# Performance work log

Hardware: AMD Instinct MI355X
Metric: run time of the kernel (lower is better)

Reference implementation:

```python
import jax, jax.numpy as jnp
import numpy as np
from jax import lax

T_SCALE = 100
D_SCALE = 100
NUM_SAMPLE = 32
PER_BIN = 3
RATIO = 0.5


def _build_sample_mask(tscale=T_SCALE, dscale=D_SCALE, num_sample=NUM_SAMPLE, perbin=PER_BIN, ratio=RATIO):
    # Vectorized, bit-faithful port of BM_layer._get_interp1d_mask (incl. np.modf
    # semantics matching math.modf for negative samples).
    T, D = tscale, dscale
    total = num_sample * perbin
    s = np.arange(T, dtype=np.float64)[:, None, None]   # start index
    d = np.arange(D, dtype=np.float64)[None, :, None]   # duration index
    clen = d + 1.0
    xmin = s - ratio * clen
    plen = d + 2.0 * ratio * clen                        # sample_xmax - sample_xmin
    step = plen / (total - 1.0)
    ii = np.arange(total, dtype=np.float64)[None, None, :]
    samples = xmin + step * ii                           # [T_start, D, total]
    frac, down_f = np.modf(samples)                      # trunc-toward-zero, like math.modf
    down = down_f.astype(np.int64)
    up = np.ceil(samples).astype(np.int64)
    acc = np.zeros((T, D, num_sample, T), dtype=np.float64)  # [start, dur, bin, time]
    S, Dg, I = np.indices((T, D, total))
    Bn = I // perbin
    m = (down >= 0) & (down <= T - 1)
    np.add.at(acc, (S[m], Dg[m], Bn[m], down[m]), 1.0 - frac[m])
    m = (up >= 0) & (up <= T - 1)
    np.add.at(acc, (S[m], Dg[m], Bn[m], up[m]), frac[m])
    acc /= perbin
    valid = (np.arange(T)[:, None] + np.arange(D)[None, :]) < T  # start+dur < tscale
    acc *= valid[:, :, None, None]
    # torch layout: [time, sample, dur, start]
    return jnp.asarray(acc.transpose(3, 2, 1, 0).astype(np.float32))


def _conv2d(x, w, pad):
    return lax.conv_general_dilated(x, w, (1, 1), ((pad, pad), (pad, pad)),
                                    dimension_numbers=('NCHW', 'OIHW', 'NCHW'))


def setup_inputs() -> dict:
    key = jax.random.key(0)
    ks = jax.random.split(key, 8)
    B, C_in, T = 4, 256, T_SCALE

    def w(k, shape, fan_in):
        return jax.random.normal(k, shape, dtype=jnp.float32) * (1.0 / np.sqrt(fan_in))

    return {
        'x': jax.random.normal(ks[0], (B, C_in, T), dtype=jnp.float32),
        'w_rd': w(ks[1], (128, C_in, 3), C_in * 3),      'b_rd': jnp.zeros((128,), jnp.float32),
        'w3d': w(ks[2], (512, 128, NUM_SAMPLE), 128 * NUM_SAMPLE), 'b3d': jnp.zeros((512,), jnp.float32),
        'w2d': w(ks[3], (128, 512), 512),                 'b2d': jnp.zeros((128,), jnp.float32),
        'wf1': w(ks[4], (128, 128, 3, 3), 128 * 9),       'bf1': jnp.zeros((128,), jnp.float32),
        'wf2': w(ks[5], (128, 128, 3, 3), 128 * 9),       'bf2': jnp.zeros((128,), jnp.float32),
        'wf3': w(ks[6], (2, 128), 128),                   'bf3': jnp.zeros((2,), jnp.float32),
        'sample_mask': _build_sample_mask(),
    }


def reference(x, w_rd, b_rd, w3d, b3d, w2d, b2d, wf1, bf1, wf2, bf2, wf3, bf3, sample_mask):
    # reduce_dim: Conv1d(256->128, k=3, pad=1) + ReLU
    h = lax.conv_general_dilated(x, w_rd, (1,), ((1, 1),),
                                 dimension_numbers=('NCH', 'OIH', 'NCH'))
    h = jax.nn.relu(h + b_rd[None, :, None])                       # [B,128,T]
    # tensordot over time axis against fixed interpolation mask
    map_base = jnp.einsum('bct,tsdu->bcsdu', h, sample_mask)       # [B,128,32,D,T]
    # conv3d with kernel (32,1,1) stride (32,1,1) == contraction over (c, s)
    m3 = jax.nn.relu(jnp.einsum('bcsdu,ocs->bodu', map_base, w3d) + b3d[None, :, None, None])
    # 1x1 conv2d 512->128
    m2 = jax.nn.relu(jnp.einsum('bodu,ko->bkdu', m3, w2d) + b2d[None, :, None, None])
    # PEM.fc head
    f = jax.nn.relu(_conv2d(m2, wf1, 1) + bf1[None, :, None, None])
    f = jax.nn.relu(_conv2d(f, wf2, 1) + bf2[None, :, None, None])
    out = jax.nn.sigmoid(jnp.einsum('bchw,kc->bkhw', f, wf3) + bf3[None, :, None, None])
    return out  # [B, 2, D, T]
```

## Files before the change

### kernel.cpp

```cpp
#include <hip/hip_runtime.h>
#include <hip/hip_bf16.h>
#include <cstdint>
#include <cstddef>

static constexpr int B   = 4;
static constexpr int CIN = 256;
static constexpr int T   = 100;
static constexpr int D   = 100;
static constexpr int S   = 32;
static constexpr int C1  = 128;
static constexpr int DU  = D * T;

typedef __attribute__((ext_vector_type(8))) short bfv8;
typedef __attribute__((ext_vector_type(4))) short bfv4;
typedef __attribute__((ext_vector_type(4))) float fx4;
typedef unsigned short us;

static __device__ __forceinline__ unsigned short f2bf(float f) {
    unsigned int x = __float_as_uint(f);
    x += 0x7FFFu + ((x >> 16) & 1u);
    return (unsigned short)(x >> 16);
}
static __device__ __forceinline__ unsigned int pk2(float a, float b) {
    return (unsigned int)f2bf(a) | ((unsigned int)f2bf(b) << 16);
}

#define MFMA16(A, Bq, C) __builtin_amdgcn_mfma_f32_16x16x32_bf16((A), (Bq), (C), 0, 0, 0)

static __device__ __forceinline__ void gload16(const void* g, void* l) {
    __builtin_amdgcn_global_load_lds(
        (const __attribute__((address_space(1))) void*)g,
        (__attribute__((address_space(3))) void*)l, 16, 0, 0);
}

__global__ __launch_bounds__(256)
void kFront(const float* __restrict__ w3d, us* __restrict__ w3B,
            const float* __restrict__ w2d, us* __restrict__ w2b,
            const float* __restrict__ wf1, us* __restrict__ wfb1,
            const float* __restrict__ wf2, us* __restrict__ wfb2,
            const float* __restrict__ x,  const float* __restrict__ wrd,
            const float* __restrict__ brd, us* __restrict__ hT,
            const float* __restrict__ mask, us* __restrict__ maskW) {
    __shared__ float wl[2][CIN * 3];
    int bid = blockIdx.x;
    int t = threadIdx.x;
    if (bid < 8192) {
        int tid = bid * 256 + t;
        int c = tid & 127;
        int o = (tid >> 7) & 511;
        int s = tid >> 16;
        w3B[tid] = f2bf(w3d[(o * 128 + c) * 32 + s]);
        return;
    }
    if (bid < 8448) {
        int tid = (bid - 8192) * 256 + t;
        w2b[tid] = f2bf(w2d[tid]);
        return;
    }
    if (bid < 9024) {
        int tid = (bid - 8448) * 256 + t;
        int c   = tid & 127;
        int k   = (tid >> 7) & 127;
        int tap = tid >> 14;
        wfb1[tid] = f2bf(wf1[(size_t)(k * 128 + c) * 9 + tap]);
        return;
    }
    if (bid < 9600) {
        int tid = (bid - 9024) * 256 + t;
        int c   = tid & 127;
        int k   = (tid >> 7) & 127;
        int tap = tid >> 14;
        wfb2[tid] = f2bf(wf2[(size_t)(k * 128 + c) * 9 + tap]);
        return;
    }
    if (bid < 9856) {
        int j = bid - 9600;
        int b  = j >> 6;
        int op = j & 63;
        int half = t >> 7;
        int lt   = t & 127;
        int o = op * 2 + half;
        for (int i = lt; i < CIN * 3; i += 128)
            wl[half][i] = wrd[o * CIN * 3 + i];
        __syncthreads();
        int tt = lt;
        float val = 0.f;
        if (tt < T) {
            float acc = brd[o];
            const float* xb = x + (size_t)b * CIN * T;
            for (int c = 0; c < CIN; ++c) {
                float xm = (tt > 0)     ? xb[c * T + tt - 1] : 0.f;
                float x0 =                xb[c * T + tt];
                float xp = (tt < T - 1) ? xb[c * T + tt + 1] : 0.f;
                acc = fmaf(wl[half][c * 3 + 0], xm, acc);
                acc = fmaf(wl[half][c * 3 + 1], x0, acc);
                acc = fmaf(wl[half][c * 3 + 2], xp, acc);
            }
            val = fmaxf(acc, 0.f);
        }
        hT[((size_t)b * 128 + tt) * 128 + o] = f2bf(val);
        return;
    }
    {
        int mb = bid - 9856;
        int ut = mb % 7;
        int dq = (mb / 7) % 25;
        int s  = mb / 175;
        int dd = t >> 6;
        int l  = t & 63;
        int l15 = l & 15, lg = l >> 4;
        int u0 = ut * 16;
        int d0 = dq * 4;

        float fs1 = (float)(3 * s), fs2 = (float)(3 * s + 2);
        float pmin = 1e30f, pmax = -1e30f;
#pragma unroll
        for (int j = 0; j < 4; ++j) {
            float dj = (float)(d0 + j);
            float step = (2.f * dj + 1.f) * (1.f / 95.f);
            float xoff = -0.5f * (dj + 1.f);
            pmin = fminf(pmin, xoff + fs1 * step);
            pmax = fmaxf(pmax, xoff + fs2 * step);
        }
        float pminT = (float)u0 + pmin;
        float pmaxT = (float)(u0 + 15) + pmax;
        bool skip = (pminT > 100.01f) || (pmaxT < -1.01f);
        int t0 = (int)floorf(pminT) - 1;
        if (t0 < 0) t0 = 0;
        t0 &= ~3;
        if (t0 > 96) t0 = 96;

        int u = u0 + l15;
        int d = d0 + dd;
        float v[8];
#pragma unroll
        for (int j = 0; j < 8; ++j) {
            int tt = t0 + lg * 8 + j;
            v[j] = 0.f;
            if (!skip && tt < 100 && u < 100)
                v[j] = mask[(((size_t)tt * 32 + s) * 100 + d) * 100 + u];
        }
        uint4 pk;
        pk.x = pk2(v[0], v[1]); pk.y = pk2(v[2], v[3]);
        pk.z = pk2(v[4], v[5]); pk.w = pk2(v[6], v[7]);
        *(uint4*)(maskW + (size_t)mb * 2048 + t * 8) = pk;
    }
}

__global__ __launch_bounds__(256, 2)
void kQm(const us* __restrict__ w3B, const us* __restrict__ hT,
         us* __restrict__ QT) {
    int bid = blockIdx.x;
    int oh = bid & 1;
    int s  = (bid >> 1) & 31;
    int b  = bid >> 6;
    int tid = threadIdx.x;
    int w   = tid >> 6;
    int l   = tid & 63;
    int l15 = l & 15, lg = l >> 4;
    int obase = oh * 256 + w * 64;
    fx4 acc[4][8];
#pragma unroll
    for (int m = 0; m < 4; ++m)
#pragma unroll
        for (int n = 0; n < 8; ++n) acc[m][n] = (fx4){0.f, 0.f, 0.f, 0.f};

#pragma unroll
    for (int ks = 0; ks < 4; ++ks) {
        int kofs = ks * 32 + lg * 8;
        bfv8 a0 = *(const bfv8*)(w3B + (size_t)(s * 512 + obase + 0 * 16 + l15) * 128 + kofs);
        bfv8 a1 = *(const bfv8*)(w3B + (size_t)(s * 512 + obase + 1 * 16 + l15) * 128 + kofs);
        bfv8 a2 = *(const bfv8*)(w3B + (size_t)(s * 512 + obase + 2 * 16 + l15) * 128 + kofs);
        bfv8 a3 = *(const bfv8*)(w3B + (size_t)(s * 512 + obase + 3 * 16 + l15) * 128 + kofs);
#pragma unroll
        for (int n = 0; n < 8; ++n) {
            bfv8 bq = *(const bfv8*)(hT + (size_t)(b * 128 + n * 16 + l15) * 128 + kofs);
            acc[0][n] = MFMA16(a0, bq, acc[0][n]);
            acc[1][n] = MFMA16(a1, bq, acc[1][n]);
            acc[2][n] = MFMA16(a2, bq, acc[2][n]);
            acc[3][n] = MFMA16(a3, bq, acc[3][n]);
        }
    }
    us* outb = QT + (size_t)(b * 32 + s) * 512 * 128;
#pragma unroll
    for (int m = 0; m < 4; ++m)
#pragma unroll
        for (int n = 0; n < 8; ++n)
#pragma unroll
            for (int r = 0; r < 4; ++r) {
                int o = obase + m * 16 + lg * 4 + r;
                outb[(size_t)o * 128 + n * 16 + l15] = f2bf(acc[m][n][r]);
            }
}

__global__ __launch_bounds__(128, 4)
void kM3m(const us* __restrict__ maskW, const us* __restrict__ QT,
          const float* __restrict__ b3d, us* __restrict__ m3b) {
    __shared__ int sl[32];
    __shared__ int nsh;
    int bid = blockIdx.x;
    int x  = bid & 7;
    int b  = x >> 1;
    int ohalf = x & 1;
    int i  = bid >> 3;
    int dq = i / 14;
    int r2 = i % 14;
    int ut = r2 >> 1;
    int os = r2 & 1;
    int u0 = ut * 16;
    int d0 = dq * 4;
    int tid = threadIdx.x;
    int w   = tid >> 6;
    int l   = tid & 63;
    int l15 = l & 15, lg = l >> 4;
    int obase = ohalf * 256 + os * 128 + w * 64;

    if (tid < 64) {
        int s = tid;
        float fs1 = (float)(3 * s), fs2 = (float)(3 * s + 2);
        float pmin = 1e30f, pmax = -1e30f;
#pragma unroll
        for (int j = 0; j < 4; ++j) {
            float dj = (float)(d0 + j);
            float step = (2.f * dj + 1.f) * (1.f / 95.f);
            float xoff = -0.5f * (dj + 1.f);
            pmin = fminf(pmin, xoff + fs1 * step);
            pmax = fmaxf(pmax, xoff + fs2 * step);
        }
        float pminT = (float)u0 + pmin;
        float pmaxT = (float)(u0 + 15) + pmax;
        bool valid = (s < 32) && !((pminT > 100.01f) || (pmaxT < -1.01f));
        int t0 = (int)floorf(pminT) - 1;
        if (t0 < 0) t0 = 0;
        t0 &= ~3;
        if (t0 > 96) t0 = 96;
        unsigned long long mb = __ballot(valid);
        int rank = __popcll(mb & ((1ull << tid) - 1ull));
        if (valid) sl[rank] = (t0 << 8) | s;
        if (tid == 0) nsh = (int)__popcll(mb);
    }
    __syncthreads();
    int ns = nsh;

    fx4 acc[4][4];
#pragma unroll
    for (int m = 0; m < 4; ++m)
#pragma unroll
        for (int n = 0; n < 4; ++n) acc[m][n] = (fx4){0.f, 0.f, 0.f, 0.f};

    const us* QTb = QT + (size_t)b * 32 * 65536
                       + (size_t)(obase + l15) * 128 + lg * 8;
    const us* mwBase = maskW + (size_t)(dq * 7 + ut) * 2048 + l * 8;

    for (int si = 0; si < ns; ++si) {
        int pk = sl[si];
        int s_ = pk & 255, t0_ = pk >> 8;
        const us* mw = mwBase + (size_t)s_ * 358400;
        bfv8 A0 = *(const bfv8*)(mw);
        bfv8 A1 = *(const bfv8*)(mw + 512);
        bfv8 A2 = *(const bfv8*)(mw + 1024);
        bfv8 A3 = *(const bfv8*)(mw + 1536);
        const us* qs = QTb + (size_t)s_ * 65536 + t0_;
        bfv4 b0l = *(const bfv4*)(qs);        bfv4 b0h = *(const bfv4*)(qs + 4);
        bfv4 b1l = *(const bfv4*)(qs + 2048); bfv4 b1h = *(const bfv4*)(qs + 2052);
        bfv4 b2l = *(const bfv4*)(qs + 4096); bfv4 b2h = *(const bfv4*)(qs + 4100);
        bfv4 b3l = *(const bfv4*)(qs + 6144); bfv4 b3h = *(const bfv4*)(qs + 6148);
        bfv8 B0 = __builtin_shufflevector(b0l, b0h, 0, 1, 2, 3, 4, 5, 6, 7);
        bfv8 B1 = __builtin_shufflevector(b1l, b1h, 0, 1, 2, 3, 4, 5, 6, 7);
        bfv8 B2 = __builtin_shufflevector(b2l, b2h, 0, 1, 2, 3, 4, 5, 6, 7);
        bfv8 B3 = __builtin_shufflevector(b3l, b3h, 0, 1, 2, 3, 4, 5, 6, 7);
        __builtin_amdgcn_s_setprio(1);
        acc[0][0] = MFMA16(A0, B0, acc[0][0]);  acc[1][0] = MFMA16(A1, B0, acc[1][0]);
        acc[2][0] = MFMA16(A2, B0, acc[2][0]);  acc[3][0] = MFMA16(A3, B0, acc[3][0]);
        acc[0][1] = MFMA16(A0, B1, acc[0][1]);  acc[1][1] = MFMA16(A1, B1, acc[1][1]);
        acc[2][1] = MFMA16(A2, B1, acc[2][1]);  acc[3][1] = MFMA16(A3, B1, acc[3][1]);
        acc[0][2] = MFMA16(A0, B2, acc[0][2]);  acc[1][2] = MFMA16(A1, B2, acc[1][2]);
        acc[2][2] = MFMA16(A2, B2, acc[2][2]);  acc[3][2] = MFMA16(A3, B2, acc[3][2]);
        acc[0][3] = MFMA16(A0, B3, acc[0][3]);  acc[1][3] = MFMA16(A1, B3, acc[1][3]);
        acc[2][3] = MFMA16(A2, B3, acc[2][3]);  acc[3][3] = MFMA16(A3, B3, acc[3][3]);
        __builtin_amdgcn_s_setprio(0);
    }

#pragma unroll
    for (int dd = 0; dd < 4; ++dd) {
#pragma unroll
        for (int n = 0; n < 4; ++n) {
            int o = obase + n * 16 + l15;
            float bias = b3d[o];
#pragma unroll
            for (int r4 = 0; r4 < 4; ++r4) {
                int u = u0 + lg * 4 + r4;
                if (u < 100)
                    m3b[((size_t)b * DU + (d0 + dd) * 100 + u) * 512 + o] =
                        f2bf(fmaxf(acc[dd][n][r4] + bias, 0.f));
            }
        }
    }
}

__global__ __launch_bounds__(256, 4)
void kM2m(const us* __restrict__ m3b, const us* __restrict__ w2b,
          const float* __restrict__ b2d, us* __restrict__ m2b) {
    int blk  = blockIdx.x;
    int tile = blk % 157;
    int b    = blk / 157;
    int du0  = tile * 64;
    int tid = threadIdx.x;
    int w   = tid >> 6;
    int l   = tid & 63;
    int l15 = l & 15, lg = l >> 4;
    fx4 acc[8];
#pragma unroll
    for (int n = 0; n < 8; ++n) acc[n] = (fx4){0.f, 0.f, 0.f, 0.f};

    int dua = du0 + w * 16 + l15; if (dua > 9999) dua = 9999;
    const us* ap = m3b + ((size_t)b * DU + dua) * 512;
#pragma unroll 4
    for (int ks = 0; ks < 16; ++ks) {
        bfv8 a = *(const bfv8*)(ap + ks * 32 + lg * 8);
#pragma unroll
        for (int n = 0; n < 8; ++n) {
            bfv8 bq = *(const bfv8*)(w2b + (size_t)(n * 16 + l15) * 512 + ks * 32 + lg * 8);
            acc[n] = MFMA16(a, bq, acc[n]);
        }
    }
#pragma unroll
    for (int n = 0; n < 8; ++n) {
        int k = n * 16 + l15;
        float bias = b2d[k];
#pragma unroll
        for (int r = 0; r < 4; ++r) {
            int du = du0 + w * 16 + lg * 4 + r;
            if (du < DU)
                m2b[((size_t)b * DU + du) * 128 + k] = f2bf(fmaxf(acc[n][r] + bias, 0.f));
        }
    }
}

template<int HEAD>
__global__ __launch_bounds__(256, 2)
void kConvM(const us* __restrict__ fin, const us* __restrict__ wfb,
            const float* __restrict__ bf, us* __restrict__ fout,
            const float* __restrict__ wf3, const float* __restrict__ bf3,
            float* __restrict__ hout) {
    __shared__ us slab[6 * 18 * 128];
    __shared__ us wl2[2][8192];
    int blk = blockIdx.x;
    int ut = blk % 7;
    int dt = (blk / 7) % 25;
    int b  = blk / 175;
    int u0 = ut * 16, d0 = dt * 4;
    int tid = threadIdx.x;
    int w   = tid >> 6;
    int l   = tid & 63;
    int l15 = l & 15, lg = l >> 4;
    fx4 acc[8];
#pragma unroll
    for (int n = 0; n < 8; ++n) acc[n] = (fx4){0.f, 0.f, 0.f, 0.f};

#define STAGE_W(BUF, P)                                                        \
    {   const int tap_ = (P) >> 1, ch_ = (P) & 1;                              \
        const us* wsrc = wfb + (size_t)tap_ * 16384 + ch_ * 64;                \
        _Pragma("unroll")                                                      \
        for (int rr = 0; rr < 4; ++rr) {                                       \
            int seg = rr * 4 + w;                                              \
            int off = seg * 1024 + l * 16;                                     \
            int k_ = off >> 7, cb_ = off & 127;                                \
            int cbs = cb_ ^ ((k_ & 7) << 4);                                   \
            gload16(wsrc + (size_t)k_ * 128 + (cbs >> 1),                      \
                    (char*)&wl2[BUF][0] + seg * 1024);                         \
        }                                                                      \
    }

    for (int i = tid; i < 1728; i += 256) {
        int cc = i & 15;
        int uu = (i >> 4) % 18;
        int dd = (i >> 4) / 18;
        int dr = d0 - 1 + dd, su = u0 - 1 + uu;
        uint4 v = {0u, 0u, 0u, 0u};
        if (dr >= 0 && dr < 100 && su >= 0 && su < 100)
            v = *(const uint4*)(fin + ((size_t)b * DU + dr * 100 + su) * 128 + cc * 8);
        int byte = (dd * 18 + uu) * 256 + ((cc * 16) ^ ((uu & 7) << 4));
        *(uint4*)((char*)slab + byte) = v;
    }
    STAGE_W(0, 0)
    __syncthreads();

#pragma unroll
    for (int p = 0; p < 18; ++p) {
        if (p + 1 < 18) STAGE_W((p + 1) & 1, p + 1)
        const int tap = p >> 1, ch = p & 1;
        const int dy = tap / 3, dx = tap % 3;
        int uu = l15 + dx;
        int ddr = w + dy;
        int arow = (ddr * 18 + uu) * 256;
        int aswz = (uu & 7) << 4;
        const char* wbuf = (const char*)&wl2[p & 1][0];
#pragma unroll
        for (int cs = 0; cs < 2; ++cs) {
            int cbyte = ch * 128 + cs * 64 + lg * 16;
            bfv8 a = *(const bfv8*)((const char*)slab + arow + (cbyte ^ aswz));
            int wcb = cs * 64 + lg * 16;
#pragma unroll
            for (int n = 0; n < 8; ++n) {
                int k = n * 16 + l15;
                bfv8 bq = *(const bfv8*)(wbuf + k * 128 + (wcb ^ ((k & 7) << 4)));
                acc[n] = MFMA16(a, bq, acc[n]);
            }
        }
        __syncthreads();
    }
#undef STAGE_W

    int d = d0 + w;
    if (HEAD == 0) {
#pragma unroll
        for (int n = 0; n < 8; ++n) {
            int k = n * 16 + l15;
            float bias = bf[k];
#pragma unroll
            for (int r = 0; r < 4; ++r) {
                int u = u0 + lg * 4 + r;
                if (u < 100)
                    fout[((size_t)b * DU + d * 100 + u) * 128 + k] =
                        f2bf(fmaxf(acc[n][r] + bias, 0.f));
            }
        }
    } else {
#pragma unroll
        for (int r = 0; r < 4; ++r) {
            float p0 = 0.f, p1 = 0.f;
#pragma unroll
            for (int n = 0; n < 8; ++n) {
                int k = n * 16 + l15;
                float f = fmaxf(acc[n][r] + bf[k], 0.f);
                p0 = fmaf(f, wf3[k], p0);
                p1 = fmaf(f, wf3[128 + k], p1);
            }
            p0 += __shfl_xor(p0, 1); p0 += __shfl_xor(p0, 2);
            p0 += __shfl_xor(p0, 4); p0 += __shfl_xor(p0, 8);
            p1 += __shfl_xor(p1, 1); p1 += __shfl_xor(p1, 2);
            p1 += __shfl_xor(p1, 4); p1 += __shfl_xor(p1, 8);
            int u = u0 + lg * 4 + r;
            if (l15 == 0 && u < 100) {
                int du = d * 100 + u;
                hout[((size_t)b * 2 + 0) * DU + du] = 1.f / (1.f + expf(-(p0 + bf3[0])));
                hout[((size_t)b * 2 + 1) * DU + du] = 1.f / (1.f + expf(-(p1 + bf3[1])));
            }
        }
    }
}

extern "C" void kernel_launch(void* const* d_in, const int* in_sizes, int n_in,
                              void* d_out, int out_size, void* d_ws, size_t ws_size,
                              hipStream_t stream) {
    const float* x    = (const float*)d_in[0];
    const float* wrd  = (const float*)d_in[1];
    const float* brd  = (const float*)d_in[2];
    const float* w3d  = (const float*)d_in[3];
    const float* b3d  = (const float*)d_in[4];
    const float* w2d  = (const float*)d_in[5];
    const float* b2d  = (const float*)d_in[6];
    const float* wf1  = (const float*)d_in[7];
    const float* bf1  = (const float*)d_in[8];
    const float* wf2  = (const float*)d_in[9];
    const float* bf2  = (const float*)d_in[10];
    const float* wf3  = (const float*)d_in[11];
    const float* bf3  = (const float*)d_in[12];
    const float* mask = (const float*)d_in[13];

    float* ws = (float*)d_ws;
    us* hT    = (us*)(ws + 0);
    us* w3B   = (us*)(ws + 32768);
    us* w2b   = (us*)(ws + 1081344);
    us* wfb1  = (us*)(ws + 1114112);
    us* wfb2  = (us*)(ws + 1187840);
    us* QT    = (us*)(ws + 1261568);
    us* maskW = (us*)(ws + 5455872);
    us* m2b   = (us*)(ws + 5455872);
    us* f1b   = (us*)(ws + 8015872);
    us* m3b   = (us*)(ws + 11190272);

    kFront<<<15456, 256, 0, stream>>>(w3d, w3B, w2d, w2b, wf1, wfb1, wf2, wfb2,
                                      x, wrd, brd, hT, mask, maskW);
    kQm<<<256, 256, 0, stream>>>(w3B, hT, QT);
    kM3m<<<2800, 128, 0, stream>>>(maskW, QT, b3d, m3b);
    kM2m<<<B * 157, 256, 0, stream>>>(m3b, w2b, b2d, m2b);
    kConvM<0><<<B * 25 * 7, 256, 0, stream>>>(m2b, wfb1, bf1, f1b,
                                              nullptr, nullptr, nullptr);
    kConvM<1><<<B * 25 * 7, 256, 0, stream>>>(f1b, wfb2, bf2, nullptr,
                                              wf3, bf3, (float*)d_out);
}
```

Before: 282.3 us.

## Software-pipeline global loads in kM3m with inline-asm double buffering

Replaces the simple per-sample loop in the m3 kernel with a two-stage software pipeline. Global loads for the next sample, issued via inline asm, overlap with the MFMA computation of the current sample, and vmcnt waits plus scheduling barriers enforce ordering. A sentinel entry in the sample list keeps the lookahead load in bounds. Launch bounds drop from 4 to 3 waves per SIMD to make room for the extra live registers, which may lower occupancy.

```diff
diff --git a/kernel.cpp b/kernel.cpp
--- a/kernel.cpp
+++ b/kernel.cpp
@@ -193,10 +193,10 @@
             }
 }
 
-__global__ __launch_bounds__(128, 4)
+__global__ __launch_bounds__(128, 3)
 void kM3m(const us* __restrict__ maskW, const us* __restrict__ QT,
           const float* __restrict__ b3d, us* __restrict__ m3b) {
-    __shared__ int sl[32];
+    __shared__ int sl[33];
     __shared__ int nsh;
     int bid = blockIdx.x;
     int x  = bid & 7;
@@ -237,7 +237,11 @@
         unsigned long long mb = __ballot(valid);
         int rank = __popcll(mb & ((1ull << tid) - 1ull));
         if (valid) sl[rank] = (t0 << 8) | s;
-        if (tid == 0) nsh = (int)__popcll(mb);
+        if (tid == 0) {
+            int n = (int)__popcll(mb);
+            nsh = n;
+            sl[n] = 0;
+        }
     }
     __syncthreads();
     int ns = nsh;
@@ -252,34 +256,73 @@
                        + (size_t)(obase + l15) * 128 + lg * 8;
     const us* mwBase = maskW + (size_t)(dq * 7 + ut) * 2048 + l * 8;
 
-    for (int si = 0; si < ns; ++si) {
-        int pk = sl[si];
-        int s_ = pk & 255, t0_ = pk >> 8;
-        const us* mw = mwBase + (size_t)s_ * 358400;
-        bfv8 A0 = *(const bfv8*)(mw);
-        bfv8 A1 = *(const bfv8*)(mw + 512);
-        bfv8 A2 = *(const bfv8*)(mw + 1024);
-        bfv8 A3 = *(const bfv8*)(mw + 1536);
-        const us* qs = QTb + (size_t)s_ * 65536 + t0_;
-        bfv4 b0l = *(const bfv4*)(qs);        bfv4 b0h = *(const bfv4*)(qs + 4);
-        bfv4 b1l = *(const bfv4*)(qs + 2048); bfv4 b1h = *(const bfv4*)(qs + 2052);
-        bfv4 b2l = *(const bfv4*)(qs + 4096); bfv4 b2h = *(const bfv4*)(qs + 4100);
-        bfv4 b3l = *(const bfv4*)(qs + 6144); bfv4 b3h = *(const bfv4*)(qs + 6148);
-        bfv8 B0 = __builtin_shufflevector(b0l, b0h, 0, 1, 2, 3, 4, 5, 6, 7);
-        bfv8 B1 = __builtin_shufflevector(b1l, b1h, 0, 1, 2, 3, 4, 5, 6, 7);
-        bfv8 B2 = __builtin_shufflevector(b2l, b2h, 0, 1, 2, 3, 4, 5, 6, 7);
-        bfv8 B3 = __builtin_shufflevector(b3l, b3h, 0, 1, 2, 3, 4, 5, 6, 7);
-        __builtin_amdgcn_s_setprio(1);
-        acc[0][0] = MFMA16(A0, B0, acc[0][0]);  acc[1][0] = MFMA16(A1, B0, acc[1][0]);
-        acc[2][0] = MFMA16(A2, B0, acc[2][0]);  acc[3][0] = MFMA16(A3, B0, acc[3][0]);
-        acc[0][1] = MFMA16(A0, B1, acc[0][1]);  acc[1][1] = MFMA16(A1, B1, acc[1][1]);
-        acc[2][1] = MFMA16(A2, B1, acc[2][1]);  acc[3][1] = MFMA16(A3, B1, acc[3][1]);
-        acc[0][2] = MFMA16(A0, B2, acc[0][2]);  acc[1][2] = MFMA16(A1, B2, acc[1][2]);
-        acc[2][2] = MFMA16(A2, B2, acc[2][2]);  acc[3][2] = MFMA16(A3, B2, acc[3][2]);
-        acc[0][3] = MFMA16(A0, B3, acc[0][3]);  acc[1][3] = MFMA16(A1, B3, acc[1][3]);
-        acc[2][3] = MFMA16(A2, B3, acc[2][3]);  acc[3][3] = MFMA16(A3, B3, acc[3][3]);
-        __builtin_amdgcn_s_setprio(0);
-    }
+#define ISSUE(SA0, SA1, SA2, SA3, S0l, S0h, S1l, S1h, S2l, S2h, S3l, S3h, PK)  \
+    {   int s_ = (PK) & 255, t0_ = (PK) >> 8;                                  \
+        const char* mA_ = (const char*)(mwBase + (size_t)s_ * 358400);         \
+        const char* q0_ = (const char*)(QTb + (size_t)s_ * 65536 + t0_);       \
+        const char* q1_ = q0_ + 4096;                                          \
+        const char* q2_ = q0_ + 8192;                                          \
+        const char* q3_ = q0_ + 12288;                                         \
+        asm volatile("global_load_dwordx4 %0, %1, off"             : "=v"(SA0) : "v"(mA_)); \
+        asm volatile("global_load_dwordx4 %0, %1, off offset:1024" : "=v"(SA1) : "v"(mA_)); \
+        asm volatile("global_load_dwordx4 %0, %1, off offset:2048" : "=v"(SA2) : "v"(mA_)); \
+        asm volatile("global_load_dwordx4 %0, %1, off offset:3072" : "=v"(SA3) : "v"(mA_)); \
+        asm volatile("global_load_dwordx2 %0, %1, off"             : "=v"(S0l) : "v"(q0_)); \
+        asm volatile("global_load_dwordx2 %0, %1, off offset:8"    : "=v"(S0h) : "v"(q0_)); \
+        asm volatile("global_load_dwordx2 %0, %1, off"             : "=v"(S1l) : "v"(q1_)); \
+        asm volatile("global_load_dwordx2 %0, %1, off offset:8"    : "=v"(S1h) : "v"(q1_)); \
+        asm volatile("global_load_dwordx2 %0, %1, off"             : "=v"(S2l) : "v"(q2_)); \
+        asm volatile("global_load_dwordx2 %0, %1, off offset:8"    : "=v"(S2h) : "v"(q2_)); \
+        asm volatile("global_load_dwordx2 %0, %1, off"             : "=v"(S3l) : "v"(q3_)); \
+        asm volatile("global_load_dwordx2 %0, %1, off offset:8"    : "=v"(S3h) : "v"(q3_)); \
+    }
+
+#define COMP(SA0, SA1, SA2, SA3, S0l, S0h, S1l, S1h, S2l, S2h, S3l, S3h)       \
+    {   bfv8 B0 = __builtin_shufflevector(S0l, S0h, 0, 1, 2, 3, 4, 5, 6, 7);   \
+        bfv8 B1 = __builtin_shufflevector(S1l, S1h, 0, 1, 2, 3, 4, 5, 6, 7);   \
+        bfv8 B2 = __builtin_shufflevector(S2l, S2h, 0, 1, 2, 3, 4, 5, 6, 7);   \
+        bfv8 B3 = __builtin_shufflevector(S3l, S3h, 0, 1, 2, 3, 4, 5, 6, 7);   \
+        __builtin_amdgcn_s_setprio(1);                                         \
+        acc[0][0] = MFMA16(SA0, B0, acc[0][0]);  acc[1][0] = MFMA16(SA1, B0, acc[1][0]); \
+        acc[2][0] = MFMA16(SA2, B0, acc[2][0]);  acc[3][0] = MFMA16(SA3, B0, acc[3][0]); \
+        acc[0][1] = MFMA16(SA0, B1, acc[0][1]);  acc[1][1] = MFMA16(SA1, B1, acc[1][1]); \
+        acc[2][1] = MFMA16(SA2, B1, acc[2][1]);  acc[3][1] = MFMA16(SA3, B1, acc[3][1]); \
+        acc[0][2] = MFMA16(SA0, B2, acc[0][2]);  acc[1][2] = MFMA16(SA1, B2, acc[1][2]); \
+        acc[2][2] = MFMA16(SA2, B2, acc[2][2]);  acc[3][2] = MFMA16(SA3, B2, acc[3][2]); \
+        acc[0][3] = MFMA16(SA0, B3, acc[0][3]);  acc[1][3] = MFMA16(SA1, B3, acc[1][3]); \
+        acc[2][3] = MFMA16(SA2, B3, acc[2][3]);  acc[3][3] = MFMA16(SA3, B3, acc[3][3]); \
+        __builtin_amdgcn_s_setprio(0);                                         \
+    }
+
+#define WAIT12()                                                               \
+    asm volatile("s_waitcnt vmcnt(12)" ::: "memory");                          \
+    __builtin_amdgcn_sched_barrier(0);
+
+    if (ns > 0) {
+        bfv8 eA0, eA1, eA2, eA3;  bfv4 e0l, e0h, e1l, e1h, e2l, e2h, e3l, e3h;
+        bfv8 oA0, oA1, oA2, oA3;  bfv4 o0l, o0h, o1l, o1h, o2l, o2h, o3l, o3h;
+        ISSUE(eA0, eA1, eA2, eA3, e0l, e0h, e1l, e1h, e2l, e2h, e3l, e3h, sl[0])
+        for (int si = 0; si < ns; si += 2) {
+            ISSUE(oA0, oA1, oA2, oA3, o0l, o0h, o1l, o1h, o2l, o2h, o3l, o3h,
+                  sl[si + 1])
+            WAIT12()
+            COMP(eA0, eA1, eA2, eA3, e0l, e0h, e1l, e1h, e2l, e2h, e3l, e3h)
+            {
+                int nx = si + 2; if (nx > ns) nx = ns;
+                ISSUE(eA0, eA1, eA2, eA3, e0l, e0h, e1l, e1h, e2l, e2h, e3l, e3h,
+                      sl[nx])
+            }
+            if (si + 1 < ns) {
+                WAIT12()
+                COMP(oA0, oA1, oA2, oA3, o0l, o0h, o1l, o1h, o2l, o2h, o3l, o3h)
+            }
+        }
+        asm volatile("s_waitcnt vmcnt(0)" ::: "memory");
+        __builtin_amdgcn_sched_barrier(0);
+    }
+#undef ISSUE
+#undef COMP
+#undef WAIT12
 
 #pragma unroll
     for (int dd = 0; dd < 4; ++dd) {
```

Measured after the change: 346.1 us. 1.23x slower.
